# Performance work log

Hardware: AMD Instinct MI355X
Metric: run time of the kernel (lower is better)

Reference implementation:

```python
import jax, jax.numpy as jnp
import numpy as np

TEMPERATURE = 8.0  # sqrt(d_k) with d_k = 64
MASK_FILL = -65504.0  # fp16 min, as in the original


def setup_inputs() -> dict:
    key = jax.random.key(0)
    kq, kk, kv, km = jax.random.split(key, 4)
    BH, L, D = 16, 2048, 64
    q = jax.random.normal(kq, (BH, L, D), dtype=jnp.float32)
    k = jax.random.normal(kk, (BH, L, D), dtype=jnp.float32)
    v = jax.random.normal(kv, (BH, L, D), dtype=jnp.float32)
    mask = jax.random.randint(km, (BH, L, L), 0, 2).astype(jnp.bool_)
    return {"q": q, "k": k, "v": v, "mask": mask}


def reference(q, k, v, mask):
    # attn = q @ k^T / temperature, masked_fill, softmax over last dim
    attn = jnp.einsum("bqd,bkd->bqk", q, k) / TEMPERATURE
    attn = jnp.where(mask, MASK_FILL, attn)
    attn = jax.nn.softmax(attn, axis=2)
    # dropout with p=0.0 is identity (eval-mode reference)
    output = jnp.einsum("bqk,bkd->bqd", attn, v)
    return (output, attn)
```

## Files before the change

### kernel.cpp

```cpp
#include <hip/hip_runtime.h>

#define BH 16
#define L 2048
#define D 64
#define QB 32
#define KB 64
#define NKT (L / KB)
#define SCALE 0.125f
#define MASK_FILL -65504.0f

typedef __bf16 bf16x8 __attribute__((ext_vector_type(8)));
typedef float f32x4 __attribute__((ext_vector_type(4)));

__device__ __forceinline__ unsigned f2bf(float f) {
    union { float f; unsigned u; } x; x.f = f;
    return (x.u + 0x7FFFu + ((x.u >> 16) & 1u)) >> 16;
}
__device__ __forceinline__ float bf2f(unsigned short h) {
    union { unsigned u; float f; } x; x.u = ((unsigned)h) << 16;
    return x.f;
}

__device__ __forceinline__ void gload16(const void* g, void* l) {
    __builtin_amdgcn_global_load_lds(
        (const __attribute__((address_space(1))) unsigned int*)g,
        (__attribute__((address_space(3))) unsigned int*)l, 16, 0, 0);
}


extern "C" __global__ __launch_bounds__(256)
void preK(const float* __restrict__ k, uint4* __restrict__ wsK)
{
    int idx = blockIdx.x * 256 + threadIdx.x;
    int c   = idx & 7;
    int key = (idx >> 3) & (L - 1);
    int bh  = idx >> 14;
    const float4* src = (const float4*)(k + ((size_t)(bh * L + key) * D + c * 8));
    float4 a = src[0], b = src[1];
    uint4 o;
    o.x = f2bf(a.x) | (f2bf(a.y) << 16);
    o.y = f2bf(a.z) | (f2bf(a.w) << 16);
    o.z = f2bf(b.x) | (f2bf(b.y) << 16);
    o.w = f2bf(b.z) | (f2bf(b.w) << 16);
    wsK[(size_t)(bh * L + key) * 8 + (c ^ (key & 7))] = o;
}

extern "C" __global__ __launch_bounds__(256)
void preV(const float* __restrict__ v, uint4* __restrict__ wsVt)
{
    __shared__ float sT[64 * 68];
    int b = blockIdx.x;
    int bh = b >> 5, kt = b & 31;
    const float4* src = (const float4*)(v + ((size_t)bh * L + kt * 64) * D);
    int t = threadIdx.x;
    #pragma unroll
    for (int i = 0; i < 4; ++i) {
        int i4 = i * 256 + t;
        int key = i4 >> 4, c4 = i4 & 15;
        float4 val = src[i4];
        *(float4*)&sT[key * 68 + c4 * 4] = val;
    }
    __syncthreads();
    int d = t >> 2, cg = t & 3;
    #pragma unroll
    for (int j = 0; j < 2; ++j) {
        int c = cg + j * 4;
        unsigned pk[4];
        #pragma unroll
        for (int e = 0; e < 4; ++e) {
            float x0 = sT[(c * 8 + e * 2    ) * 68 + d];
            float x1 = sT[(c * 8 + e * 2 + 1) * 68 + d];
            pk[e] = f2bf(x0) | (f2bf(x1) << 16);
        }
        wsVt[((size_t)(bh * 32 + kt) * 64 + d) * 8 + (c ^ (d & 7))] =
            make_uint4(pk[0], pk[1], pk[2], pk[3]);
    }
}

extern "C" __global__ __launch_bounds__(256)
void preM(const int* __restrict__ mask, unsigned long long* __restrict__ wsM)
{
    __shared__ unsigned long long sW[16 * 32];
    int b = blockIdx.x;
    size_t row0 = (size_t)b * 16;
    int w = threadIdx.x >> 6, lane = threadIdx.x & 63;
    const int* src = mask + row0 * L;
    for (int rr = 0; rr < 4; ++rr) {
        int r = w * 4 + rr;
        #pragma unroll 8
        for (int wd = 0; wd < 32; ++wd) {
            int val = src[(size_t)r * L + wd * 64 + lane];
            unsigned long long bal = __ballot(val != 0);
            if (lane == 0) sW[r * 32 + wd] = bal;
        }
    }
    __syncthreads();
    int t = threadIdx.x;
    ((uint4*)wsM)[(size_t)b * 256 + t] = ((const uint4*)sW)[t];
}


extern "C" __global__ __launch_bounds__(256, 4)
void sdpa_main(const float* __restrict__ q, const uint4* __restrict__ gKall,
               const uint4* __restrict__ gVall, const unsigned long long* __restrict__ wsM,
               float* __restrict__ out, float* __restrict__ attn)
{
    __shared__ unsigned short sK[2][KB * 64];
    __shared__ unsigned short sVt[2][D * 64];
    __shared__ unsigned short sP[QB * 72];
    __shared__ float sPart[4][16];

    const int tid = threadIdx.x, lane = tid & 63, w = tid >> 6;
    const int wr = w & 1, wn = w >> 1;
    const int quad = lane >> 4, l15 = lane & 15;
    const int p = blockIdx.x, bh = p & 15, qb = p >> 4, q0 = qb * QB;

    const uint4* gK = gKall + (size_t)bh * L * 8;
    const uint4* gV = gVall + (size_t)bh * L * 8;

    const float* Qp = q + (size_t)(bh * L + q0 + wr * 16 + l15) * D + quad * 8;
    float4 qv0 = *(const float4*)(Qp);
    float4 qv1 = *(const float4*)(Qp + 4);
    float4 qv2 = *(const float4*)(Qp + 32);
    float4 qv3 = *(const float4*)(Qp + 36);
    union { bf16x8 v; unsigned short s[8]; } qa0u, qa1u;
    qa0u.s[0] = f2bf(qv0.x); qa0u.s[1] = f2bf(qv0.y); qa0u.s[2] = f2bf(qv0.z); qa0u.s[3] = f2bf(qv0.w);
    qa0u.s[4] = f2bf(qv1.x); qa0u.s[5] = f2bf(qv1.y); qa0u.s[6] = f2bf(qv1.z); qa0u.s[7] = f2bf(qv1.w);
    qa1u.s[0] = f2bf(qv2.x); qa1u.s[1] = f2bf(qv2.y); qa1u.s[2] = f2bf(qv2.z); qa1u.s[3] = f2bf(qv2.w);
    qa1u.s[4] = f2bf(qv3.x); qa1u.s[5] = f2bf(qv3.y); qa1u.s[6] = f2bf(qv3.z); qa1u.s[7] = f2bf(qv3.w);
    const bf16x8 qa0 = qa0u.v, qa1 = qa1u.v;

    const unsigned long long* Mw = wsM + (size_t)(bh * L + q0 + wr * 16 + quad * 4) * 32;

    auto stageK = [&](int kt, int buf) {
        const uint4* s = gK + (size_t)kt * 512 + w * 128 + lane;
        gload16(s,      &sK[buf][(w * 128) * 8]);
        gload16(s + 64, &sK[buf][(w * 128 + 64) * 8]);
    };
    auto stageV = [&](int kt, int buf) {
        const uint4* s = gV + (size_t)kt * 512 + w * 128 + lane;
        gload16(s,      &sVt[buf][(w * 128) * 8]);
        gload16(s + 64, &sVt[buf][(w * 128 + 64) * 8]);
    };
    auto scompute = [&](int cur, f32x4* acc) {
        #pragma unroll
        for (int j = 0; j < 2; ++j) {
            int key = (wn * 2 + j) * 16 + l15;
            const bf16x8 b0 = *(const bf16x8*)&sK[cur][key * 64 + ((quad     ^ (key & 7)) * 8)];
            const bf16x8 b1 = *(const bf16x8*)&sK[cur][key * 64 + (((quad+4) ^ (key & 7)) * 8)];
            f32x4 c = {0.f, 0.f, 0.f, 0.f};
            c = __builtin_amdgcn_mfma_f32_16x16x32_bf16(qa0, b0, c, 0, 0, 0);
            c = __builtin_amdgcn_mfma_f32_16x16x32_bf16(qa1, b1, c, 0, 0, 0);
            acc[j] = c;
        }
    };

    float lsum[4] = {0.f, 0.f, 0.f, 0.f};
    stageK(0, 0);
    __syncthreads();
    for (int kt = 0; kt < NKT; ++kt) {
        int cur = kt & 1;
        if (kt + 1 < NKT) stageK(kt + 1, cur ^ 1);
        unsigned long long mw[4];
        #pragma unroll
        for (int r = 0; r < 4; ++r) mw[r] = Mw[r * 32 + kt];
        f32x4 acc[2];
        scompute(cur, acc);
        #pragma unroll
        for (int j = 0; j < 2; ++j) {
            int sh = (wn * 2 + j) * 16 + l15;
            #pragma unroll
            for (int r = 0; r < 4; ++r) {
                float val = acc[j][r] * SCALE;
                val = ((mw[r] >> sh) & 1ull) ? MASK_FILL : val;
                lsum[r] += __expf(val);
            }
        }
        __syncthreads();
    }
    #pragma unroll
    for (int off = 1; off < 16; off <<= 1)
        #pragma unroll
        for (int r = 0; r < 4; ++r) lsum[r] += __shfl_xor(lsum[r], off, 64);
    if (l15 == 0) {
        #pragma unroll
        for (int r = 0; r < 4; ++r) sPart[w][quad * 4 + r] = lsum[r];
    }
    __syncthreads();
    float rinv[4];
    #pragma unroll
    for (int r = 0; r < 4; ++r)
        rinv[r] = 1.0f / (sPart[wr][quad * 4 + r] + sPart[wr + 2][quad * 4 + r]);

    f32x4 oacc[2];
    oacc[0] = (f32x4){0.f, 0.f, 0.f, 0.f};
    oacc[1] = (f32x4){0.f, 0.f, 0.f, 0.f};
    float* Ab = attn + ((size_t)bh * L + q0) * L;

    stageK(0, 0); stageV(0, 0);
    __syncthreads();
    for (int kt = 0; kt < NKT; ++kt) {
        int cur = kt & 1;
        if (kt + 1 < NKT) { stageK(kt + 1, cur ^ 1); stageV(kt + 1, cur ^ 1); }
        unsigned long long mw[4];
        #pragma unroll
        for (int r = 0; r < 4; ++r) mw[r] = Mw[r * 32 + kt];
        f32x4 acc[2];
        scompute(cur, acc);
        #pragma unroll
        for (int j = 0; j < 2; ++j) {
            int col = (wn * 2 + j) * 16 + l15;
            #pragma unroll
            for (int r = 0; r < 4; ++r) {
                float val = acc[j][r] * SCALE;
                val = ((mw[r] >> col) & 1ull) ? MASK_FILL : val;
                float pr = __expf(val) * rinv[r];
                int row = wr * 16 + quad * 4 + r;
                Ab[(size_t)row * L + kt * 64 + col] = pr;
                sP[row * 72 + col] = (unsigned short)f2bf(pr);
            }
        }
        __syncthreads();
        {
            const bf16x8 pa0 = *(const bf16x8*)&sP[(wr * 16 + l15) * 72 + quad * 8];
            const bf16x8 pa1 = *(const bf16x8*)&sP[(wr * 16 + l15) * 72 + quad * 8 + 32];
            #pragma unroll
            for (int j = 0; j < 2; ++j) {
                int dd = (wn * 2 + j) * 16 + l15;
                const bf16x8 vb0 = *(const bf16x8*)&sVt[cur][dd * 64 + ((quad     ^ (dd & 7)) * 8)];
                const bf16x8 vb1 = *(const bf16x8*)&sVt[cur][dd * 64 + (((quad+4) ^ (dd & 7)) * 8)];
                oacc[j] = __builtin_amdgcn_mfma_f32_16x16x32_bf16(pa0, vb0, oacc[j], 0, 0, 0);
                oacc[j] = __builtin_amdgcn_mfma_f32_16x16x32_bf16(pa1, vb1, oacc[j], 0, 0, 0);
            }
        }
        __syncthreads();
    }

    float* Ob = out + ((size_t)bh * L + q0) * D;
    #pragma unroll
    for (int j = 0; j < 2; ++j)
        #pragma unroll
        for (int r = 0; r < 4; ++r)
            Ob[(size_t)(wr * 16 + quad * 4 + r) * D + (wn * 2 + j) * 16 + l15] = oacc[j][r];
}


extern "C" __global__ __launch_bounds__(256, 2)
void sdpa_kernel(const float* __restrict__ q, const float* __restrict__ k,
                 const float* __restrict__ v, const int* __restrict__ mask,
                 float* __restrict__ out, float* __restrict__ attn)
{
    __shared__ unsigned short fQ[64 * 72];
    __shared__ unsigned short fK[64 * 72];
    __shared__ unsigned short fVt[64 * 72];
    __shared__ unsigned short fP[64 * 72];
    __shared__ unsigned long long fM[64 * 33];

    const int tid  = threadIdx.x;
    const int lane = tid & 63;
    const int w    = tid >> 6;
    const int quad = lane >> 4;
    const int l15  = lane & 15;

    const int p  = blockIdx.x;
    const int bh = p & (BH - 1);
    const int qb = p >> 4;
    const int q0 = qb * 64;

    const size_t base = (size_t)bh * L * D;
    const float* Qb = q + base + (size_t)q0 * D;
    const float* Kb = k + base;
    const float* Vb = v + base;
    const int*   Mb = mask + (size_t)bh * L * L + (size_t)q0 * L;
    float*       Ab = attn + (size_t)bh * L * L + (size_t)q0 * L;
    float*       Ob = out  + base + (size_t)q0 * D;

    {
        const float2* Qs = (const float2*)Qb;
        for (int i = 0; i < 8; ++i) {
            int idx = i * 256 + tid;
            int row = idx >> 5, d2 = idx & 31;
            float2 val = Qs[idx];
            unsigned pk = f2bf(val.x) | (f2bf(val.y) << 16);
            *(unsigned*)&fQ[row * 72 + d2 * 2] = pk;
        }
    }
    for (int rr = 0; rr < 16; ++rr) {
        int row = w * 16 + rr;
        const int4* Ms = (const int4*)(Mb + (size_t)row * L);
        for (int it = 0; it < 8; ++it) {
            int4 mv = Ms[it * 64 + lane];
            unsigned long long b0 = __ballot(mv.x != 0);
            unsigned long long b1 = __ballot(mv.y != 0);
            unsigned long long b2 = __ballot(mv.z != 0);
            unsigned long long b3 = __ballot(mv.w != 0);
            if (lane == 0) {
                unsigned long long* dst = &fM[row * 33 + it * 4];
                dst[0] = b0; dst[1] = b1; dst[2] = b2; dst[3] = b3;
            }
        }
    }
    __syncthreads();

    const int qrow = w * 16 + l15;
    bf16x8 qa0 = *(const bf16x8*)&fQ[qrow * 72 + quad * 8];
    bf16x8 qa1 = *(const bf16x8*)&fQ[qrow * 72 + quad * 8 + 32];

    float lsum[4] = {0.f, 0.f, 0.f, 0.f};
    for (int kt = 0; kt < 32; ++kt) {
        const int k0 = kt * 64;
        __syncthreads();
        {
            const float2* Ks = (const float2*)(Kb + (size_t)k0 * D);
            for (int i = 0; i < 8; ++i) {
                int idx = i * 256 + tid;
                int row = idx >> 5, d2 = idx & 31;
                float2 val = Ks[idx];
                unsigned pk = f2bf(val.x) | (f2bf(val.y) << 16);
                *(unsigned*)&fK[row * 72 + d2 * 2] = pk;
            }
        }
        __syncthreads();
        f32x4 acc[4];
        for (int nt = 0; nt < 4; ++nt) {
            bf16x8 b0 = *(const bf16x8*)&fK[(nt * 16 + l15) * 72 + quad * 8];
            bf16x8 b1 = *(const bf16x8*)&fK[(nt * 16 + l15) * 72 + quad * 8 + 32];
            f32x4 c = {0.f, 0.f, 0.f, 0.f};
            c = __builtin_amdgcn_mfma_f32_16x16x32_bf16(qa0, b0, c, 0, 0, 0);
            c = __builtin_amdgcn_mfma_f32_16x16x32_bf16(qa1, b1, c, 0, 0, 0);
            acc[nt] = c;
        }
        const int widx = (k0 >> 8) * 4 + (lane & 3);
        const int bsh0 = (k0 >> 2) + (l15 >> 2);
        for (int r = 0; r < 4; ++r) {
            int row = w * 16 + quad * 4 + r;
            unsigned long long mwv = fM[row * 33 + widx];
            float s = 0.f;
            for (int nt = 0; nt < 4; ++nt) {
                float val = acc[nt][r] * SCALE;
                int bit = (int)((mwv >> ((bsh0 + nt * 4) & 63)) & 1ull);
                val = bit ? MASK_FILL : val;
                s += __expf(val);
            }
            lsum[r] += s;
        }
    }
    for (int off = 1; off < 16; off <<= 1)
        for (int r = 0; r < 4; ++r) lsum[r] += __shfl_xor(lsum[r], off, 64);
    float rinv[4];
    for (int r = 0; r < 4; ++r) rinv[r] = 1.0f / lsum[r];

    f32x4 oacc[4];
    for (int nt = 0; nt < 4; ++nt) oacc[nt] = (f32x4){0.f, 0.f, 0.f, 0.f};

    for (int kt = 0; kt < 32; ++kt) {
        const int k0 = kt * 64;
        __syncthreads();
        {
            const float2* Ks = (const float2*)(Kb + (size_t)k0 * D);
            for (int i = 0; i < 8; ++i) {
                int idx = i * 256 + tid;
                int row = idx >> 5, d2 = idx & 31;
                float2 val = Ks[idx];
                unsigned pk = f2bf(val.x) | (f2bf(val.y) << 16);
                *(unsigned*)&fK[row * 72 + d2 * 2] = pk;
            }
        }
        {
            unsigned pk[8];
            for (int jj = 0; jj < 16; ++jj) {
                float val = Vb[(size_t)(k0 + w * 16 + jj) * D + lane];
                unsigned bv = f2bf(val);
                if (jj & 1) pk[jj >> 1] |= bv << 16;
                else        pk[jj >> 1]  = bv;
            }
            uint4* dst = (uint4*)&fVt[lane * 72 + w * 16];
            dst[0] = make_uint4(pk[0], pk[1], pk[2], pk[3]);
            dst[1] = make_uint4(pk[4], pk[5], pk[6], pk[7]);
        }
        __syncthreads();
        f32x4 acc[4];
        for (int nt = 0; nt < 4; ++nt) {
            bf16x8 b0 = *(const bf16x8*)&fK[(nt * 16 + l15) * 72 + quad * 8];
            bf16x8 b1 = *(const bf16x8*)&fK[(nt * 16 + l15) * 72 + quad * 8 + 32];
            f32x4 c = {0.f, 0.f, 0.f, 0.f};
            c = __builtin_amdgcn_mfma_f32_16x16x32_bf16(qa0, b0, c, 0, 0, 0);
            c = __builtin_amdgcn_mfma_f32_16x16x32_bf16(qa1, b1, c, 0, 0, 0);
            acc[nt] = c;
        }
        const int widx = (k0 >> 8) * 4 + (lane & 3);
        const int bsh0 = (k0 >> 2) + (l15 >> 2);
        for (int r = 0; r < 4; ++r) {
            int row = w * 16 + quad * 4 + r;
            unsigned long long mwv = fM[row * 33 + widx];
            for (int nt = 0; nt < 4; ++nt) {
                float val = acc[nt][r] * SCALE;
                int bit = (int)((mwv >> ((bsh0 + nt * 4) & 63)) & 1ull);
                val = bit ? MASK_FILL : val;
                float pr = __expf(val) * rinv[r];
                fP[row * 72 + nt * 16 + l15] = (unsigned short)f2bf(pr);
            }
        }
        for (int it = 0; it < 4; ++it) {
            int row = w * 16 + it * 4 + quad;
            unsigned long long pv = *(const unsigned long long*)&fP[row * 72 + l15 * 4];
            float4 o;
            o.x = bf2f((unsigned short)(pv         & 0xFFFF));
            o.y = bf2f((unsigned short)((pv >> 16) & 0xFFFF));
            o.z = bf2f((unsigned short)((pv >> 32) & 0xFFFF));
            o.w = bf2f((unsigned short)((pv >> 48) & 0xFFFF));
            *(float4*)&Ab[(size_t)row * L + k0 + l15 * 4] = o;
        }
        {
            bf16x8 pa0 = *(const bf16x8*)&fP[qrow * 72 + quad * 8];
            bf16x8 pa1 = *(const bf16x8*)&fP[qrow * 72 + quad * 8 + 32];
            for (int nt = 0; nt < 4; ++nt) {
                bf16x8 vb0 = *(const bf16x8*)&fVt[(nt * 16 + l15) * 72 + quad * 8];
                bf16x8 vb1 = *(const bf16x8*)&fVt[(nt * 16 + l15) * 72 + quad * 8 + 32];
                oacc[nt] = __builtin_amdgcn_mfma_f32_16x16x32_bf16(pa0, vb0, oacc[nt], 0, 0, 0);
                oacc[nt] = __builtin_amdgcn_mfma_f32_16x16x32_bf16(pa1, vb1, oacc[nt], 0, 0, 0);
            }
        }
    }
    for (int nt = 0; nt < 4; ++nt)
        for (int r = 0; r < 4; ++r)
            Ob[(size_t)(w * 16 + quad * 4 + r) * D + nt * 16 + l15] = oacc[nt][r];
}


extern "C" void kernel_launch(void* const* d_in, const int* in_sizes, int n_in,
                              void* d_out, int out_size, void* d_ws, size_t ws_size,
                              hipStream_t stream)
{
    const float* q    = (const float*)d_in[0];
    const float* k    = (const float*)d_in[1];
    const float* v    = (const float*)d_in[2];
    const int*   mask = (const int*)d_in[3];
    float* out  = (float*)d_out;
    float* attn = out + (size_t)BH * L * D;

    const size_t WS_K  = 0;
    const size_t WS_VT = (size_t)BH * L * D * 2;
    const size_t WS_M  = WS_VT + (size_t)BH * L * D * 2;
    const size_t NEED  = WS_M + (size_t)BH * L * 32 * 8;

    if (ws_size >= NEED) {
        uint4* wsK  = (uint4*)((char*)d_ws + WS_K);
        uint4* wsVt = (uint4*)((char*)d_ws + WS_VT);
        unsigned long long* wsM = (unsigned long long*)((char*)d_ws + WS_M);
        hipLaunchKernelGGL(preK, dim3(1024), dim3(256), 0, stream, k, wsK);
        hipLaunchKernelGGL(preV, dim3(512),  dim3(256), 0, stream, v, wsVt);
        hipLaunchKernelGGL(preM, dim3(2048), dim3(256), 0, stream, mask, wsM);
        hipLaunchKernelGGL(sdpa_main, dim3(BH * (L / QB)), dim3(256), 0, stream,
                           q, (const uint4*)wsK, (const uint4*)wsVt, wsM, out, attn);
    } else {
        hipLaunchKernelGGL(sdpa_kernel, dim3(BH * (L / 64)), dim3(256), 0, stream,
                           q, k, v, mask, out, attn);
    }
}
```

Measured before the change: 605.7 us.

## Drop mask prepass and LDS staging; load K/V fragments directly into registers

Removes the preM kernel that packed the mask into bitwords. The main kernel now reads the int mask directly in the first pass and keeps per-thread bits in registers for the second pass. K and V fragments are loaded straight from global memory into MFMA operand registers with a one-tile register prefetch, replacing global-to-LDS staging and its barriers. sP is double-buffered so each tile needs one barrier instead of two. The trade-off is uncoalesced 16-byte global loads, heavier K/V traffic that relies on the cache, and strided int mask reads.

```diff
diff --git a/kernel.cpp b/kernel.cpp
--- a/kernel.cpp
+++ b/kernel.cpp
@@ -19,12 +19,6 @@
 __device__ __forceinline__ float bf2f(unsigned short h) {
     union { unsigned u; float f; } x; x.u = ((unsigned)h) << 16;
     return x.f;
-}
-
-__device__ __forceinline__ void gload16(const void* g, void* l) {
-    __builtin_amdgcn_global_load_lds(
-        (const __attribute__((address_space(1))) unsigned int*)g,
-        (__attribute__((address_space(3))) unsigned int*)l, 16, 0, 0);
 }
 
 
@@ -77,37 +71,13 @@
     }
 }
 
-extern "C" __global__ __launch_bounds__(256)
-void preM(const int* __restrict__ mask, unsigned long long* __restrict__ wsM)
-{
-    __shared__ unsigned long long sW[16 * 32];
-    int b = blockIdx.x;
-    size_t row0 = (size_t)b * 16;
-    int w = threadIdx.x >> 6, lane = threadIdx.x & 63;
-    const int* src = mask + row0 * L;
-    for (int rr = 0; rr < 4; ++rr) {
-        int r = w * 4 + rr;
-        #pragma unroll 8
-        for (int wd = 0; wd < 32; ++wd) {
-            int val = src[(size_t)r * L + wd * 64 + lane];
-            unsigned long long bal = __ballot(val != 0);
-            if (lane == 0) sW[r * 32 + wd] = bal;
-        }
-    }
-    __syncthreads();
-    int t = threadIdx.x;
-    ((uint4*)wsM)[(size_t)b * 256 + t] = ((const uint4*)sW)[t];
-}
-
 
 extern "C" __global__ __launch_bounds__(256, 4)
 void sdpa_main(const float* __restrict__ q, const uint4* __restrict__ gKall,
-               const uint4* __restrict__ gVall, const unsigned long long* __restrict__ wsM,
+               const uint4* __restrict__ gVall, const int* __restrict__ mask,
                float* __restrict__ out, float* __restrict__ attn)
 {
-    __shared__ unsigned short sK[2][KB * 64];
-    __shared__ unsigned short sVt[2][D * 64];
-    __shared__ unsigned short sP[QB * 72];
+    __shared__ unsigned short sP[2][QB * 72];
     __shared__ float sPart[4][16];
 
     const int tid = threadIdx.x, lane = tid & 63, w = tid >> 6;
@@ -130,54 +100,83 @@
     qa1u.s[4] = f2bf(qv3.x); qa1u.s[5] = f2bf(qv3.y); qa1u.s[6] = f2bf(qv3.z); qa1u.s[7] = f2bf(qv3.w);
     const bf16x8 qa0 = qa0u.v, qa1 = qa1u.v;
 
-    const unsigned long long* Mw = wsM + (size_t)(bh * L + q0 + wr * 16 + quad * 4) * 32;
-
-    auto stageK = [&](int kt, int buf) {
-        const uint4* s = gK + (size_t)kt * 512 + w * 128 + lane;
-        gload16(s,      &sK[buf][(w * 128) * 8]);
-        gload16(s + 64, &sK[buf][(w * 128 + 64) * 8]);
+    const int key0 = wn * 32 + l15;
+    const int key1 = key0 + 16;
+    const int s7 = l15 & 7;
+    const int o00 = key0 * 8 + ((quad    ) ^ s7);
+    const int o01 = key0 * 8 + ((quad + 4) ^ s7);
+    const int o10 = key1 * 8 + ((quad    ) ^ s7);
+    const int o11 = key1 * 8 + ((quad + 4) ^ s7);
+
+    auto loadK = [&](int kt, bf16x8& a, bf16x8& b, bf16x8& c, bf16x8& d) {
+        const uint4* base = gK + (size_t)kt * 512;
+        a = *(const bf16x8*)(base + o00);
+        b = *(const bf16x8*)(base + o01);
+        c = *(const bf16x8*)(base + o10);
+        d = *(const bf16x8*)(base + o11);
     };
-    auto stageV = [&](int kt, int buf) {
-        const uint4* s = gV + (size_t)kt * 512 + w * 128 + lane;
-        gload16(s,      &sVt[buf][(w * 128) * 8]);
-        gload16(s + 64, &sVt[buf][(w * 128 + 64) * 8]);
+    auto loadV = [&](int kt, bf16x8& a, bf16x8& b, bf16x8& c, bf16x8& d) {
+        const uint4* base = gV + (size_t)kt * 512;
+        a = *(const bf16x8*)(base + o00);
+        b = *(const bf16x8*)(base + o01);
+        c = *(const bf16x8*)(base + o10);
+        d = *(const bf16x8*)(base + o11);
     };
-    auto scompute = [&](int cur, f32x4* acc) {
+
+    const int* Mb0 = mask + ((size_t)bh * L + q0 + wr * 16 + quad * 4) * L
+                          + wn * 32 + l15;
+
+    unsigned mb[8] = {0u, 0u, 0u, 0u, 0u, 0u, 0u, 0u};
+
+    float lsum[4] = {0.f, 0.f, 0.f, 0.f};
+
+    bf16x8 k0c, k1c, k2c, k3c;
+    loadK(0, k0c, k1c, k2c, k3c);
+    int mc[8];
+    #pragma unroll
+    for (int r = 0; r < 4; ++r) {
+        mc[2 * r]     = Mb0[(size_t)r * L];
+        mc[2 * r + 1] = Mb0[(size_t)r * L + 16];
+    }
+
+    for (int kt = 0; kt < NKT; ++kt) {
+        bf16x8 k0n, k1n, k2n, k3n;
+        int mn[8];
+        const bool pf = (kt + 1 < NKT);
+        if (pf) {
+            loadK(kt + 1, k0n, k1n, k2n, k3n);
+            const int* mrow = Mb0 + (kt + 1) * 64;
+            #pragma unroll
+            for (int r = 0; r < 4; ++r) {
+                mn[2 * r]     = mrow[(size_t)r * L];
+                mn[2 * r + 1] = mrow[(size_t)r * L + 16];
+            }
+        }
+        f32x4 acc[2];
+        acc[0] = (f32x4){0.f, 0.f, 0.f, 0.f};
+        acc[0] = __builtin_amdgcn_mfma_f32_16x16x32_bf16(qa0, k0c, acc[0], 0, 0, 0);
+        acc[0] = __builtin_amdgcn_mfma_f32_16x16x32_bf16(qa1, k1c, acc[0], 0, 0, 0);
+        acc[1] = (f32x4){0.f, 0.f, 0.f, 0.f};
+        acc[1] = __builtin_amdgcn_mfma_f32_16x16x32_bf16(qa0, k2c, acc[1], 0, 0, 0);
+        acc[1] = __builtin_amdgcn_mfma_f32_16x16x32_bf16(qa1, k3c, acc[1], 0, 0, 0);
         #pragma unroll
         for (int j = 0; j < 2; ++j) {
-            int key = (wn * 2 + j) * 16 + l15;
-            const bf16x8 b0 = *(const bf16x8*)&sK[cur][key * 64 + ((quad     ^ (key & 7)) * 8)];
-            const bf16x8 b1 = *(const bf16x8*)&sK[cur][key * 64 + (((quad+4) ^ (key & 7)) * 8)];
-            f32x4 c = {0.f, 0.f, 0.f, 0.f};
-            c = __builtin_amdgcn_mfma_f32_16x16x32_bf16(qa0, b0, c, 0, 0, 0);
-            c = __builtin_amdgcn_mfma_f32_16x16x32_bf16(qa1, b1, c, 0, 0, 0);
-            acc[j] = c;
-        }
-    };
-
-    float lsum[4] = {0.f, 0.f, 0.f, 0.f};
-    stageK(0, 0);
-    __syncthreads();
-    for (int kt = 0; kt < NKT; ++kt) {
-        int cur = kt & 1;
-        if (kt + 1 < NKT) stageK(kt + 1, cur ^ 1);
-        unsigned long long mw[4];
-        #pragma unroll
-        for (int r = 0; r < 4; ++r) mw[r] = Mw[r * 32 + kt];
-        f32x4 acc[2];
-        scompute(cur, acc);
-        #pragma unroll
-        for (int j = 0; j < 2; ++j) {
-            int sh = (wn * 2 + j) * 16 + l15;
             #pragma unroll
             for (int r = 0; r < 4; ++r) {
                 float val = acc[j][r] * SCALE;
-                val = ((mw[r] >> sh) & 1ull) ? MASK_FILL : val;
+                const bool m = (mc[2 * r + j] != 0);
+                mb[2 * r + j] |= (m ? (1u << kt) : 0u);
+                val = m ? MASK_FILL : val;
                 lsum[r] += __expf(val);
             }
         }
-        __syncthreads();
-    }
+        if (pf) {
+            k0c = k0n; k1c = k1n; k2c = k2n; k3c = k3n;
+            #pragma unroll
+            for (int i = 0; i < 8; ++i) mc[i] = mn[i];
+        }
+    }
+
     #pragma unroll
     for (int off = 1; off < 16; off <<= 1)
         #pragma unroll
@@ -197,43 +196,41 @@
     oacc[1] = (f32x4){0.f, 0.f, 0.f, 0.f};
     float* Ab = attn + ((size_t)bh * L + q0) * L;
 
-    stageK(0, 0); stageV(0, 0);
-    __syncthreads();
+    loadK(0, k0c, k1c, k2c, k3c);
     for (int kt = 0; kt < NKT; ++kt) {
-        int cur = kt & 1;
-        if (kt + 1 < NKT) { stageK(kt + 1, cur ^ 1); stageV(kt + 1, cur ^ 1); }
-        unsigned long long mw[4];
-        #pragma unroll
-        for (int r = 0; r < 4; ++r) mw[r] = Mw[r * 32 + kt];
         f32x4 acc[2];
-        scompute(cur, acc);
+        acc[0] = (f32x4){0.f, 0.f, 0.f, 0.f};
+        acc[0] = __builtin_amdgcn_mfma_f32_16x16x32_bf16(qa0, k0c, acc[0], 0, 0, 0);
+        acc[0] = __builtin_amdgcn_mfma_f32_16x16x32_bf16(qa1, k1c, acc[0], 0, 0, 0);
+        acc[1] = (f32x4){0.f, 0.f, 0.f, 0.f};
+        acc[1] = __builtin_amdgcn_mfma_f32_16x16x32_bf16(qa0, k2c, acc[1], 0, 0, 0);
+        acc[1] = __builtin_amdgcn_mfma_f32_16x16x32_bf16(qa1, k3c, acc[1], 0, 0, 0);
+
+        unsigned short* sPb = sP[kt & 1];
         #pragma unroll
         for (int j = 0; j < 2; ++j) {
-            int col = (wn * 2 + j) * 16 + l15;
+            const int col = key0 + j * 16;
             #pragma unroll
             for (int r = 0; r < 4; ++r) {
                 float val = acc[j][r] * SCALE;
-                val = ((mw[r] >> col) & 1ull) ? MASK_FILL : val;
+                val = ((mb[2 * r + j] >> kt) & 1u) ? MASK_FILL : val;
                 float pr = __expf(val) * rinv[r];
-                int row = wr * 16 + quad * 4 + r;
+                const int row = wr * 16 + quad * 4 + r;
                 Ab[(size_t)row * L + kt * 64 + col] = pr;
-                sP[row * 72 + col] = (unsigned short)f2bf(pr);
+                sPb[row * 72 + col] = (unsigned short)f2bf(pr);
             }
         }
         __syncthreads();
-        {
-            const bf16x8 pa0 = *(const bf16x8*)&sP[(wr * 16 + l15) * 72 + quad * 8];
-            const bf16x8 pa1 = *(const bf16x8*)&sP[(wr * 16 + l15) * 72 + quad * 8 + 32];
-            #pragma unroll
-            for (int j = 0; j < 2; ++j) {
-                int dd = (wn * 2 + j) * 16 + l15;
-                const bf16x8 vb0 = *(const bf16x8*)&sVt[cur][dd * 64 + ((quad     ^ (dd & 7)) * 8)];
-                const bf16x8 vb1 = *(const bf16x8*)&sVt[cur][dd * 64 + (((quad+4) ^ (dd & 7)) * 8)];
-                oacc[j] = __builtin_amdgcn_mfma_f32_16x16x32_bf16(pa0, vb0, oacc[j], 0, 0, 0);
-                oacc[j] = __builtin_amdgcn_mfma_f32_16x16x32_bf16(pa1, vb1, oacc[j], 0, 0, 0);
-            }
-        }
-        __syncthreads();
+        if (kt + 1 < NKT) loadK(kt + 1, k0c, k1c, k2c, k3c);
+
+        const bf16x8 pa0 = *(const bf16x8*)&sPb[(wr * 16 + l15) * 72 + quad * 8];
+        const bf16x8 pa1 = *(const bf16x8*)&sPb[(wr * 16 + l15) * 72 + quad * 8 + 32];
+        bf16x8 v0, v1, v2, v3;
+        loadV(kt, v0, v1, v2, v3);
+        oacc[0] = __builtin_amdgcn_mfma_f32_16x16x32_bf16(pa0, v0, oacc[0], 0, 0, 0);
+        oacc[0] = __builtin_amdgcn_mfma_f32_16x16x32_bf16(pa1, v1, oacc[0], 0, 0, 0);
+        oacc[1] = __builtin_amdgcn_mfma_f32_16x16x32_bf16(pa0, v2, oacc[1], 0, 0, 0);
+        oacc[1] = __builtin_amdgcn_mfma_f32_16x16x32_bf16(pa1, v3, oacc[1], 0, 0, 0);
     }
 
     float* Ob = out + ((size_t)bh * L + q0) * D;
@@ -441,18 +438,15 @@
 
     const size_t WS_K  = 0;
     const size_t WS_VT = (size_t)BH * L * D * 2;
-    const size_t WS_M  = WS_VT + (size_t)BH * L * D * 2;
-    const size_t NEED  = WS_M + (size_t)BH * L * 32 * 8;
+    const size_t NEED  = WS_VT + (size_t)BH * L * D * 2;
 
     if (ws_size >= NEED) {
         uint4* wsK  = (uint4*)((char*)d_ws + WS_K);
         uint4* wsVt = (uint4*)((char*)d_ws + WS_VT);
-        unsigned long long* wsM = (unsigned long long*)((char*)d_ws + WS_M);
         hipLaunchKernelGGL(preK, dim3(1024), dim3(256), 0, stream, k, wsK);
         hipLaunchKernelGGL(preV, dim3(512),  dim3(256), 0, stream, v, wsVt);
-        hipLaunchKernelGGL(preM, dim3(2048), dim3(256), 0, stream, mask, wsM);
         hipLaunchKernelGGL(sdpa_main, dim3(BH * (L / QB)), dim3(256), 0, stream,
-                           q, (const uint4*)wsK, (const uint4*)wsVt, wsM, out, attn);
+                           q, (const uint4*)wsK, (const uint4*)wsVt, mask, out, attn);
     } else {
         hipLaunchKernelGGL(sdpa_kernel, dim3(BH * (L / 64)), dim3(256), 0, stream,
                            q, k, v, mask, out, attn);
```

After: 605.7 us. About the same (-0.0%).
